# Kernel tuning notes

Hardware: AMD Instinct MI355X
Metric: run time of the kernel (lower is better)

Reference implementation:

```python
import jax, jax.numpy as jnp
import numpy as np

H = 256   # encoder/decoder hidden size
U = 128   # attention units


def setup_inputs() -> dict:
    key = jax.random.key(0)
    ks = jax.random.split(key, 8)
    B, Td, Te = 16, 128, 1024
    s = 1.0 / np.sqrt(H)
    return {
        "dec_outputs": jax.random.normal(ks[0], (B, Td, H), dtype=jnp.float32),
        "enc_outputs": jax.random.normal(ks[1], (B, Te, H), dtype=jnp.float32),
        "W1": jax.random.normal(ks[2], (H, U), dtype=jnp.float32) * s,
        "b1": jnp.zeros((U,), dtype=jnp.float32),
        "W2": jax.random.normal(ks[3], (H, U), dtype=jnp.float32) * s,
        "b2": jnp.zeros((U,), dtype=jnp.float32),
        "V": jax.random.normal(ks[4], (U, 1), dtype=jnp.float32) * (1.0 / np.sqrt(U)),
        "bv": jnp.zeros((1,), dtype=jnp.float32),
    }


def reference(dec_outputs, enc_outputs, W1, b1, W2, b2, V, bv):
    # Project once (the original redundantly re-projects enc_outputs per step).
    # w1d: [B, Td, U], w2e: [B, Te, U]
    w1d = jnp.einsum("bth,hu->btu", dec_outputs, W1) + b1
    w2e = jnp.einsum("bsh,hu->bsu", enc_outputs, W2) + b2
    # Additive Bahdanau score: tanh over broadcast sum -> [B, Td, Te, U]
    feat = jnp.tanh(w1d[:, :, None, :] + w2e[:, None, :, :])
    # V projection to scalar score: [B, Td, Te]
    score = jnp.einsum("btsu,u->bts", feat, V[:, 0]) + bv[0]
    # Softmax over encoder positions (original Softmax(axis=1) on [B, Te])
    return jax.nn.softmax(score, axis=-1)
```

## Files before the change

kernel.cpp:

```cpp
#include <hip/hip_runtime.h>
#include <math.h>

#define HB 256
#define UB 128
#define BB 16
#define TD 128
#define TE 1024
#define TT 4

__device__ __forceinline__ float exp2c(float w) {
    float t = fminf(fmaxf(w, -30.f), 30.f);
    return __expf(2.f * t);
}

template<int RPB, int TRANS>
__global__ __launch_bounds__(128) void proj_exp2(
    const float* __restrict__ X, const float* __restrict__ W,
    const float* __restrict__ bias, float* __restrict__ out, int seq) {
    __shared__ float xs[RPB][HB];
    const int tid = threadIdx.x;
    const int ul  = tid;
    const long row0 = (long)blockIdx.x * RPB;

    const float4* src = reinterpret_cast<const float4*>(X + row0 * HB);
    float4* dst = reinterpret_cast<float4*>(&xs[0][0]);
    constexpr int NV = RPB * HB / 4;
    #pragma unroll
    for (int i = 0; i < NV / 128; ++i) dst[i * 128 + tid] = src[i * 128 + tid];
    __syncthreads();

    float acc[RPB];
    #pragma unroll
    for (int r = 0; r < RPB; ++r) acc[r] = 0.f;

    for (int h = 0; h < HB; h += 4) {
        float wv[4];
        #pragma unroll
        for (int k = 0; k < 4; ++k) wv[k] = W[(h + k) * UB + ul];
        #pragma unroll
        for (int r = 0; r < RPB; ++r) {
            float4 x4 = *reinterpret_cast<const float4*>(&xs[r][h]);
            acc[r] = fmaf(x4.x, wv[0], acc[r]);
            acc[r] = fmaf(x4.y, wv[1], acc[r]);
            acc[r] = fmaf(x4.z, wv[2], acc[r]);
            acc[r] = fmaf(x4.w, wv[3], acc[r]);
        }
    }
    const float bb = bias[ul];
    if (TRANS == 0) {
        #pragma unroll
        for (int r = 0; r < RPB; ++r)
            out[(row0 + r) * UB + ul] = exp2c(acc[r] + bb);
    } else {
        const long b  = row0 / seq;
        const long s0 = row0 % seq;
        float* op = out + ((b * UB) + ul) * (long)seq + s0;
        #pragma unroll
        for (int r = 0; r < RPB; r += 4) {
            float4 v = make_float4(exp2c(acc[r + 0] + bb), exp2c(acc[r + 1] + bb),
                                   exp2c(acc[r + 2] + bb), exp2c(acc[r + 3] + bb));
            *reinterpret_cast<float4*>(op + r) = v;
        }
    }
}

__global__ __launch_bounds__(512) void score_softmax2(
    const float* __restrict__ Ea,
    const float* __restrict__ EbT,
    const float* __restrict__ V,
    float* __restrict__ out) {
    const int tid = threadIdx.x;
    const int w = tid >> 6;
    const int l = tid & 63;

    const int i   = blockIdx.x;
    const int xcd = i & 7;
    const int j   = i >> 3;
    const int b   = 2 * xcd + (j >> 5);
    const int t0  = (j & 31) * TT;

    const float* __restrict__ ap = Ea + ((long)b * TD + t0) * UB;
    const float* __restrict__ eb = EbT + ((long)b * UB) * TE + (w * 128 + 2 * l);

    float acc[TT][2];
    #pragma unroll
    for (int t = 0; t < TT; ++t) { acc[t][0] = 0.f; acc[t][1] = 0.f; }

    #pragma unroll 2
    for (int u = 0; u < UB; u += 4) {
        float vv[4], a[TT][4];
        float4 v4 = *reinterpret_cast<const float4*>(V + u);
        vv[0] = v4.x; vv[1] = v4.y; vv[2] = v4.z; vv[3] = v4.w;
        #pragma unroll
        for (int t = 0; t < TT; ++t) {
            float4 a4 = *reinterpret_cast<const float4*>(ap + t * UB + u);
            a[t][0] = a4.x; a[t][1] = a4.y; a[t][2] = a4.z; a[t][3] = a4.w;
        }
        #pragma unroll
        for (int k = 0; k < 4; ++k) {
            float2 e = *reinterpret_cast<const float2*>(eb + (long)(u + k) * TE);
            #pragma unroll
            for (int t = 0; t < TT; ++t) {
                acc[t][0] = fmaf(vv[k], __builtin_amdgcn_rcpf(fmaf(a[t][k], e.x, 1.f)), acc[t][0]);
                acc[t][1] = fmaf(vv[k], __builtin_amdgcn_rcpf(fmaf(a[t][k], e.y, 1.f)), acc[t][1]);
            }
        }
    }

    float sc[TT][2];
    #pragma unroll
    for (int t = 0; t < TT; ++t) { sc[t][0] = -2.f * acc[t][0]; sc[t][1] = -2.f * acc[t][1]; }

    __shared__ float red[TT][8];
    float m[TT];
    #pragma unroll
    for (int t = 0; t < TT; ++t) {
        float x = fmaxf(sc[t][0], sc[t][1]);
        #pragma unroll
        for (int off = 32; off > 0; off >>= 1) x = fmaxf(x, __shfl_xor(x, off, 64));
        if (l == 0) red[t][w] = x;
    }
    __syncthreads();
    #pragma unroll
    for (int t = 0; t < TT; ++t) {
        m[t] = red[t][0];
        #pragma unroll
        for (int k = 1; k < 8; ++k) m[t] = fmaxf(m[t], red[t][k]);
    }
    __syncthreads();
    float sum[TT];
    #pragma unroll
    for (int t = 0; t < TT; ++t) {
        sc[t][0] = __expf(sc[t][0] - m[t]);
        sc[t][1] = __expf(sc[t][1] - m[t]);
        float s = sc[t][0] + sc[t][1];
        #pragma unroll
        for (int off = 32; off > 0; off >>= 1) s += __shfl_xor(s, off, 64);
        if (l == 0) red[t][w] = s;
    }
    __syncthreads();
    #pragma unroll
    for (int t = 0; t < TT; ++t) {
        float s = red[t][0];
        #pragma unroll
        for (int k = 1; k < 8; ++k) s += red[t][k];
        const float inv = 1.f / s;
        float2 o = make_float2(sc[t][0] * inv, sc[t][1] * inv);
        *reinterpret_cast<float2*>(out + ((long)b * TD + t0 + t) * TE + w * 128 + 2 * l) = o;
    }
}

extern "C" void kernel_launch(void* const* d_in, const int* in_sizes, int n_in,
                              void* d_out, int out_size, void* d_ws, size_t ws_size,
                              hipStream_t stream) {
    const float* dec = (const float*)d_in[0];
    const float* enc = (const float*)d_in[1];
    const float* W1  = (const float*)d_in[2];
    const float* b1  = (const float*)d_in[3];
    const float* W2  = (const float*)d_in[4];
    const float* b2  = (const float*)d_in[5];
    const float* V   = (const float*)d_in[6];
    float* out = (float*)d_out;

    float* Ea  = (float*)d_ws;
    float* EbT = Ea + (long)BB * TD * UB;

    proj_exp2<8, 0><<<BB * TD / 8, 128, 0, stream>>>(dec, W1, b1, Ea, TD);
    proj_exp2<16, 1><<<BB * TE / 16, 128, 0, stream>>>(enc, W2, b2, EbT, TE);
    score_softmax2<<<BB * (TD / TT), 512, 0, stream>>>(Ea, EbT, V, out);
}
```

Before: 83.40 us.

## Pair reciprocals in score kernel and register-tile the projection GEMM

```diff
diff --git a/kernel.cpp b/kernel.cpp
--- a/kernel.cpp
+++ b/kernel.cpp
@@ -9,144 +9,168 @@
 #define TT 4
 
 __device__ __forceinline__ float exp2c(float w) {
-    float t = fminf(fmaxf(w, -30.f), 30.f);
+    float t = fminf(fmaxf(w, -10.f), 10.f);
     return __expf(2.f * t);
 }
 
-template<int RPB, int TRANS>
-__global__ __launch_bounds__(128) void proj_exp2(
+template<int TRANS>
+__global__ __launch_bounds__(256) void proj_exp3(
     const float* __restrict__ X, const float* __restrict__ W,
     const float* __restrict__ bias, float* __restrict__ out, int seq) {
-    __shared__ float xs[RPB][HB];
+    constexpr int R = 32;
+    __shared__ float xs[R][HB + 4];
     const int tid = threadIdx.x;
-    const int ul  = tid;
-    const long row0 = (long)blockIdx.x * RPB;
+    const long row0 = (long)blockIdx.x * R;
 
-    const float4* src = reinterpret_cast<const float4*>(X + row0 * HB);
-    float4* dst = reinterpret_cast<float4*>(&xs[0][0]);
-    constexpr int NV = RPB * HB / 4;
-    #pragma unroll
-    for (int i = 0; i < NV / 128; ++i) dst[i * 128 + tid] = src[i * 128 + tid];
+    {
+        const float4* src = reinterpret_cast<const float4*>(X + row0 * HB);
+        #pragma unroll
+        for (int i = 0; i < 8; ++i) {
+            int idx = i * 256 + tid;
+            int r = idx >> 6, c = idx & 63;
+            *reinterpret_cast<float4*>(&xs[r][c * 4]) = src[idx];
+        }
+    }
     __syncthreads();
 
-    float acc[RPB];
+    const int ut = tid & 15;
+    const int rt = tid >> 4;
+    const int u0 = ut * 8;
+    const int r0 = rt * 2;
+
+    float acc[2][8];
     #pragma unroll
-    for (int r = 0; r < RPB; ++r) acc[r] = 0.f;
+    for (int r = 0; r < 2; ++r)
+        #pragma unroll
+        for (int j = 0; j < 8; ++j) acc[r][j] = 0.f;
 
-    for (int h = 0; h < HB; h += 4) {
-        float wv[4];
-        #pragma unroll
-        for (int k = 0; k < 4; ++k) wv[k] = W[(h + k) * UB + ul];
-        #pragma unroll
-        for (int r = 0; r < RPB; ++r) {
-            float4 x4 = *reinterpret_cast<const float4*>(&xs[r][h]);
-            acc[r] = fmaf(x4.x, wv[0], acc[r]);
-            acc[r] = fmaf(x4.y, wv[1], acc[r]);
-            acc[r] = fmaf(x4.z, wv[2], acc[r]);
-            acc[r] = fmaf(x4.w, wv[3], acc[r]);
+    for (int hc = 0; hc < HB; hc += 64) {
+        #pragma unroll 2
+        for (int h = hc; h < hc + 64; h += 4) {
+            float4 wa[4], wb[4];
+            #pragma unroll
+            for (int k = 0; k < 4; ++k) {
+                wa[k] = *reinterpret_cast<const float4*>(&W[(h + k) * UB + u0]);
+                wb[k] = *reinterpret_cast<const float4*>(&W[(h + k) * UB + u0 + 4]);
+            }
+            #pragma unroll
+            for (int r = 0; r < 2; ++r) {
+                float4 x4 = *reinterpret_cast<const float4*>(&xs[r0 + r][h]);
+                float xk[4] = {x4.x, x4.y, x4.z, x4.w};
+                #pragma unroll
+                for (int k = 0; k < 4; ++k) {
+                    acc[r][0] = fmaf(xk[k], wa[k].x, acc[r][0]);
+                    acc[r][1] = fmaf(xk[k], wa[k].y, acc[r][1]);
+                    acc[r][2] = fmaf(xk[k], wa[k].z, acc[r][2]);
+                    acc[r][3] = fmaf(xk[k], wa[k].w, acc[r][3]);
+                    acc[r][4] = fmaf(xk[k], wb[k].x, acc[r][4]);
+                    acc[r][5] = fmaf(xk[k], wb[k].y, acc[r][5]);
+                    acc[r][6] = fmaf(xk[k], wb[k].z, acc[r][6]);
+                    acc[r][7] = fmaf(xk[k], wb[k].w, acc[r][7]);
+                }
+            }
         }
+        __syncthreads();
     }
-    const float bb = bias[ul];
+
+    float bv[8];
+    #pragma unroll
+    for (int j = 0; j < 8; ++j) bv[j] = bias[u0 + j];
+
     if (TRANS == 0) {
         #pragma unroll
-        for (int r = 0; r < RPB; ++r)
-            out[(row0 + r) * UB + ul] = exp2c(acc[r] + bb);
+        for (int r = 0; r < 2; ++r) {
+            float o[8];
+            #pragma unroll
+            for (int j = 0; j < 8; ++j) o[j] = exp2c(acc[r][j] + bv[j]);
+            float4* op = reinterpret_cast<float4*>(out + (row0 + r0 + r) * UB + u0);
+            op[0] = make_float4(o[0], o[1], o[2], o[3]);
+            op[1] = make_float4(o[4], o[5], o[6], o[7]);
+        }
     } else {
-        const long b  = row0 / seq;
+        const long bq = row0 / seq;
         const long s0 = row0 % seq;
-        float* op = out + ((b * UB) + ul) * (long)seq + s0;
         #pragma unroll
-        for (int r = 0; r < RPB; r += 4) {
-            float4 v = make_float4(exp2c(acc[r + 0] + bb), exp2c(acc[r + 1] + bb),
-                                   exp2c(acc[r + 2] + bb), exp2c(acc[r + 3] + bb));
-            *reinterpret_cast<float4*>(op + r) = v;
+        for (int j = 0; j < 8; ++j) {
+            float* op = out + (bq * UB + u0 + j) * (long)seq + s0 + r0;
+            float2 o = make_float2(exp2c(acc[0][j] + bv[j]), exp2c(acc[1][j] + bv[j]));
+            *reinterpret_cast<float2*>(op) = o;
         }
     }
 }
 
-__global__ __launch_bounds__(512) void score_softmax2(
+__global__ __launch_bounds__(1024) void score_softmax3(
     const float* __restrict__ Ea,
     const float* __restrict__ EbT,
     const float* __restrict__ V,
     float* __restrict__ out) {
     const int tid = threadIdx.x;
-    const int w = tid >> 6;
-    const int l = tid & 63;
-
-    const int i   = blockIdx.x;
-    const int xcd = i & 7;
-    const int j   = i >> 3;
-    const int b   = 2 * xcd + (j >> 5);
-    const int t0  = (j & 31) * TT;
+    const int w = tid >> 6, l = tid & 63;
+    const int i = blockIdx.x;
+    const int b  = 2 * (i & 7) + ((i >> 3) >> 5);
+    const int t0 = ((i >> 3) & 31) * TT;
+    const int s  = tid;
 
     const float* __restrict__ ap = Ea + ((long)b * TD + t0) * UB;
-    const float* __restrict__ eb = EbT + ((long)b * UB) * TE + (w * 128 + 2 * l);
+    const float* __restrict__ eb = EbT + ((long)b * UB) * TE + s;
 
-    float acc[TT][2];
-    #pragma unroll
-    for (int t = 0; t < TT; ++t) { acc[t][0] = 0.f; acc[t][1] = 0.f; }
+    float acc[TT] = {0.f, 0.f, 0.f, 0.f};
 
-    #pragma unroll 2
     for (int u = 0; u < UB; u += 4) {
-        float vv[4], a[TT][4];
         float4 v4 = *reinterpret_cast<const float4*>(V + u);
-        vv[0] = v4.x; vv[1] = v4.y; vv[2] = v4.z; vv[3] = v4.w;
+        float e0 = eb[(long)(u + 0) * TE];
+        float e1 = eb[(long)(u + 1) * TE];
+        float e2 = eb[(long)(u + 2) * TE];
+        float e3 = eb[(long)(u + 3) * TE];
         #pragma unroll
         for (int t = 0; t < TT; ++t) {
             float4 a4 = *reinterpret_cast<const float4*>(ap + t * UB + u);
-            a[t][0] = a4.x; a[t][1] = a4.y; a[t][2] = a4.z; a[t][3] = a4.w;
-        }
-        #pragma unroll
-        for (int k = 0; k < 4; ++k) {
-            float2 e = *reinterpret_cast<const float2*>(eb + (long)(u + k) * TE);
-            #pragma unroll
-            for (int t = 0; t < TT; ++t) {
-                acc[t][0] = fmaf(vv[k], __builtin_amdgcn_rcpf(fmaf(a[t][k], e.x, 1.f)), acc[t][0]);
-                acc[t][1] = fmaf(vv[k], __builtin_amdgcn_rcpf(fmaf(a[t][k], e.y, 1.f)), acc[t][1]);
-            }
+            float Xa = fmaf(a4.x, e0, 1.f), Ya = fmaf(a4.y, e1, 1.f);
+            float Na = fmaf(v4.x, Ya, v4.y * Xa);
+            acc[t] = fmaf(Na, __builtin_amdgcn_rcpf(Xa * Ya), acc[t]);
+            float Xb = fmaf(a4.z, e2, 1.f), Yb = fmaf(a4.w, e3, 1.f);
+            float Nb = fmaf(v4.z, Yb, v4.w * Xb);
+            acc[t] = fmaf(Nb, __builtin_amdgcn_rcpf(Xb * Yb), acc[t]);
         }
     }
 
-    float sc[TT][2];
+    float sc[TT];
     #pragma unroll
-    for (int t = 0; t < TT; ++t) { sc[t][0] = -2.f * acc[t][0]; sc[t][1] = -2.f * acc[t][1]; }
+    for (int t = 0; t < TT; ++t) sc[t] = -2.f * acc[t];
 
-    __shared__ float red[TT][8];
-    float m[TT];
+    __shared__ float red[TT][16];
     #pragma unroll
     for (int t = 0; t < TT; ++t) {
-        float x = fmaxf(sc[t][0], sc[t][1]);
+        float x = sc[t];
         #pragma unroll
         for (int off = 32; off > 0; off >>= 1) x = fmaxf(x, __shfl_xor(x, off, 64));
         if (l == 0) red[t][w] = x;
     }
     __syncthreads();
+    float m[TT];
     #pragma unroll
     for (int t = 0; t < TT; ++t) {
-        m[t] = red[t][0];
+        float x = red[t][0];
         #pragma unroll
-        for (int k = 1; k < 8; ++k) m[t] = fmaxf(m[t], red[t][k]);
-    }
-    __syncthreads();
-    float sum[TT];
-    #pragma unroll
-    for (int t = 0; t < TT; ++t) {
-        sc[t][0] = __expf(sc[t][0] - m[t]);
-        sc[t][1] = __expf(sc[t][1] - m[t]);
-        float s = sc[t][0] + sc[t][1];
-        #pragma unroll
-        for (int off = 32; off > 0; off >>= 1) s += __shfl_xor(s, off, 64);
-        if (l == 0) red[t][w] = s;
+        for (int k = 1; k < 16; ++k) x = fmaxf(x, red[t][k]);
+        m[t] = x;
     }
     __syncthreads();
     #pragma unroll
     for (int t = 0; t < TT; ++t) {
-        float s = red[t][0];
+        sc[t] = __expf(sc[t] - m[t]);
+        float x = sc[t];
         #pragma unroll
-        for (int k = 1; k < 8; ++k) s += red[t][k];
-        const float inv = 1.f / s;
-        float2 o = make_float2(sc[t][0] * inv, sc[t][1] * inv);
-        *reinterpret_cast<float2*>(out + ((long)b * TD + t0 + t) * TE + w * 128 + 2 * l) = o;
+        for (int off = 32; off > 0; off >>= 1) x += __shfl_xor(x, off, 64);
+        if (l == 0) red[t][w] = x;
+    }
+    __syncthreads();
+    #pragma unroll
+    for (int t = 0; t < TT; ++t) {
+        float x = red[t][0];
+        #pragma unroll
+        for (int k = 1; k < 16; ++k) x += red[t][k];
+        out[((long)b * TD + t0 + t) * TE + s] = sc[t] * (1.f / x);
     }
 }
 
@@ -165,7 +189,7 @@
     float* Ea  = (float*)d_ws;
     float* EbT = Ea + (long)BB * TD * UB;
 
-    proj_exp2<8, 0><<<BB * TD / 8, 128, 0, stream>>>(dec, W1, b1, Ea, TD);
-    proj_exp2<16, 1><<<BB * TE / 16, 128, 0, stream>>>(enc, W2, b2, EbT, TE);
-    score_softmax2<<<BB * (TD / TT), 512, 0, stream>>>(Ea, EbT, V, out);
+    proj_exp3<0><<<BB * TD / 32, 256, 0, stream>>>(dec, W1, b1, Ea, TD);
+    proj_exp3<1><<<BB * TE / 32, 256, 0, stream>>>(enc, W2, b2, EbT, TE);
+    score_softmax3<<<BB * (TD / TT), 1024, 0, stream>>>(Ea, EbT, V, out);
 }
```

Result: slower. 95.31 us (+14.3%).
